# Kernel optimization log

Hardware: AMD Instinct MI355X
Metric: run time of the kernel (lower is better)

The kernel has to match this reference:

```python
import jax, jax.numpy as jnp
import numpy as np

B, S, D, H, L = 64, 512, 512, 512, 2  # batch, seq, input_size, hidden_size, num_layers


def setup_inputs() -> dict:
    key = jax.random.key(0)
    ks = jax.random.split(key, 7)
    scale = 1.0 / np.sqrt(H)  # torch LSTMCell init range
    return {
        "input": jax.random.normal(ks[0], (B, S, D), dtype=jnp.float32),
        "enc_h": jax.random.normal(ks[1], (B, H), dtype=jnp.float32),
        "enc_c": jax.random.normal(ks[2], (B, H), dtype=jnp.float32),
        "W_ih": jax.random.uniform(ks[3], (L, 4 * H, D), jnp.float32, -scale, scale),
        "W_hh": jax.random.uniform(ks[4], (L, 4 * H, H), jnp.float32, -scale, scale),
        "b_ih": jax.random.uniform(ks[5], (L, 4 * H), jnp.float32, -scale, scale),
        "b_hh": jax.random.uniform(ks[6], (L, 4 * H), jnp.float32, -scale, scale),
    }


def _lstm_cell(x, h, c, W_ih_j, W_hh_j, b_ih_j, b_hh_j):
    # PyTorch LSTMCell gate order: i, f, g, o
    gates = x @ W_ih_j.T + b_ih_j + h @ W_hh_j.T + b_hh_j  # [B, 4H]
    i, f, g, o = jnp.split(gates, 4, axis=-1)
    c_new = jax.nn.sigmoid(f) * c + jax.nn.sigmoid(i) * jnp.tanh(g)
    h_new = jax.nn.sigmoid(o) * jnp.tanh(c_new)
    return h_new, c_new


def reference(input, enc_h, enc_c, W_ih, W_hh, b_ih, b_hh):
    # encoder_out is None in this configuration, so attention is skipped;
    # all layers are initialized with (enc_h, enc_c), as in the torch code.
    h0 = jnp.broadcast_to(enc_h, (L,) + enc_h.shape)  # [L, B, H]
    c0 = jnp.broadcast_to(enc_c, (L,) + enc_c.shape)

    def step(carry, x_t):
        hs, cs = carry
        h = x_t
        new_h, new_c = [], []
        for j in range(L):  # small fixed layer loop
            h, c = _lstm_cell(h, hs[j], cs[j], W_ih[j], W_hh[j], b_ih[j], b_hh[j])
            new_h.append(h)
            new_c.append(c)
        return (jnp.stack(new_h), jnp.stack(new_c)), h

    (hs, cs), out = jax.lax.scan(step, (h0, c0), jnp.swapaxes(input, 0, 1))
    out = jnp.swapaxes(out, 0, 1)  # [B, S, H]
    return out, (hs[-1], cs[-1])
```

## Files before the change

### kernel.cpp

```cpp
#include <hip/hip_runtime.h>


#define NB 64
#define NS 512
#define ND 512
#define NH 512

typedef __attribute__((ext_vector_type(8))) short short8;
typedef __attribute__((ext_vector_type(4))) float f32x4;

#define WPK_OFF   0
#define H0_OFF    8388608
#define H1_OFF    8650752
#define FLAGS_OFF 8781824
#define WPK_ELEMS_PER_ROLE (128 * 32 * 512)

__device__ __forceinline__ unsigned int pack2bf(float a, float b) {
    unsigned int ua = __builtin_bit_cast(unsigned int, a);
    unsigned int ub = __builtin_bit_cast(unsigned int, b);
    ua += 0x7fffu + ((ua >> 16) & 1u);
    ub += 0x7fffu + ((ub >> 16) & 1u);
    return (ua >> 16) | (ub & 0xffff0000u);
}
__device__ __forceinline__ unsigned short bf16r(float a) {
    unsigned int ua = __builtin_bit_cast(unsigned int, a);
    ua += 0x7fffu + ((ua >> 16) & 1u);
    return (unsigned short)(ua >> 16);
}

__device__ __forceinline__ unsigned long long ld_h64(const void* p) {
    return __hip_atomic_load((const unsigned long long*)p, __ATOMIC_RELAXED,
                             __HIP_MEMORY_SCOPE_AGENT);
}
__device__ __forceinline__ void st_h32(void* p, unsigned int v) {
    __hip_atomic_store((unsigned int*)p, v, __ATOMIC_RELAXED,
                       __HIP_MEMORY_SCOPE_AGENT);
}
__device__ __forceinline__ unsigned int ld_flag(const unsigned int* p) {
    return __hip_atomic_load(p, __ATOMIC_RELAXED, __HIP_MEMORY_SCOPE_AGENT);
}
__device__ __forceinline__ void st_flag(unsigned int* p, unsigned int v) {
    __hip_atomic_store(p, v, __ATOMIC_RELAXED, __HIP_MEMORY_SCOPE_AGENT);
}

__global__ void prep_weights_k(const float* __restrict__ W_ih,
                               const float* __restrict__ W_hh,
                               unsigned int* __restrict__ wpk_u32) {
    long long gid = (long long)blockIdx.x * blockDim.x + threadIdx.x;
    int l   = (int)(gid & 63);
    int k0i = (int)((gid >> 6) & 31);
    int nt  = (int)((gid >> 11) & 127);
    int r   = (int)(gid >> 18);
    int n = nt * 16 + (l & 15);
    int k = k0i * 32 + ((l >> 4) << 3);
    const float* src;
    if (k < 512) src = W_ih + ((long long)r * 2048 + n) * 512 + k;
    else         src = W_hh + ((long long)r * 2048 + n) * 512 + (k - 512);
    uint4 v;
    v.x = pack2bf(src[0], src[1]);
    v.y = pack2bf(src[2], src[3]);
    v.z = pack2bf(src[4], src[5]);
    v.w = pack2bf(src[6], src[7]);
    ((uint4*)wpk_u32)[gid] = v;
}

__global__ void prep_state_k(const float* __restrict__ eh,
                             unsigned short* __restrict__ h0base,
                             unsigned short* __restrict__ h1base,
                             unsigned int* __restrict__ flags) {
    int i = blockIdx.x * blockDim.x + threadIdx.x;
    if (i < NB * NH) {
        unsigned short hb = bf16r(eh[i]);
        (h0base + 3 * 32768)[i] = hb;
        (h1base + 1 * 32768)[i] = hb;
    }
    if (i < 256) flags[i] = 0;
}

__global__ __launch_bounds__(512, 1)
void lstm_persist_k(const float* __restrict__ input,
                    const float* __restrict__ enc_c,
                    const float* __restrict__ b_ih,
                    const float* __restrict__ b_hh,
                    const unsigned short* __restrict__ wpk,
                    unsigned short* __restrict__ h0base,
                    unsigned short* __restrict__ h1base,
                    float* __restrict__ out,
                    unsigned int* __restrict__ flags) {
    __shared__ alignas(16) unsigned char smem[32768];
    __shared__ float Gp[8][16][17];
    const int bid  = blockIdx.x;
    const int role = bid >> 7;
    const int lb   = bid & 127;
    const int ms   = lb >> 5;
    const int us   = lb & 31;
    const int m0   = ms << 4;
    const int tid  = threadIdx.x;
    const int lane = tid & 63;
    const int w    = tid >> 6;
    const int g    = __builtin_amdgcn_readfirstlane(w & 3);
    const int kh   = __builtin_amdgcn_readfirstlane(w >> 2);

    const unsigned short* wp = wpk + (long long)role * WPK_ELEMS_PER_ROLE
                             + (long long)(g * 32 + us) * (32 * 512)
                             + (long long)kh * 16 * 512;
    const unsigned char* aBase = smem + kh * 16384;

    short8 wreg[16];
    #pragma unroll
    for (int j = 0; j < 16; ++j)
        wreg[j] = *(const short8*)(wp + j * 512 + lane * 8);
    #pragma unroll
    for (int j = 0; j < 16; ++j)
        asm volatile("" : "+v"(wreg[j]));

    unsigned int* myflag   = flags + (ms << 6) + (role << 5) + us;
    const unsigned int* gf = flags + (ms << 6) + lane;

    const int m_l = (tid >> 4) & 15, u_l = tid & 15;
    const int bcell = m0 + m_l;
    const int ucell = us * 16 + u_l;
    float cReg = 0.f, bias_i = 0.f, bias_f = 0.f, bias_g = 0.f, bias_o = 0.f;
    if (tid < 256) {
        cReg = enc_c[bcell * NH + ucell];
        const long long br = (long long)role * 2048;
        bias_i = b_ih[br + 0 * 512 + ucell] + b_hh[br + 0 * 512 + ucell];
        bias_f = b_ih[br + 1 * 512 + ucell] + b_hh[br + 1 * 512 + ucell];
        bias_g = b_ih[br + 2 * 512 + ucell] + b_hh[br + 2 * 512 + ucell];
        bias_o = b_ih[br + 3 * 512 + ucell] + b_hh[br + 3 * 512 + ucell];
    }

    const int srow  = tid & 15;
    const int skoff = ((tid >> 4) & 3) << 3;

    float4 xp[4];
    if (role == 0) {
        #pragma unroll
        for (int j2 = 0; j2 < 2; ++j2) {
            int sid = j2 * 512 + tid;
            int k = (sid >> 6) * 32 + skoff;
            const float* s = input + (long long)(m0 + srow) * (NS * ND) + k;
            xp[2 * j2]     = *(const float4*)s;
            xp[2 * j2 + 1] = *(const float4*)(s + 4);
        }
    }

    for (int i = 0; i <= NS; ++i) {
        const bool active = (role == 0) ? (i < NS) : (i >= 1);

        if (role == 0 && i < NS) {
            #pragma unroll
            for (int j2 = 0; j2 < 2; ++j2) {
                int sid = j2 * 512 + tid;
                float4 lo = xp[2 * j2], hi = xp[2 * j2 + 1];
                uint4 val;
                val.x = pack2bf(lo.x, lo.y);
                val.y = pack2bf(lo.z, lo.w);
                val.z = pack2bf(hi.x, hi.y);
                val.w = pack2bf(hi.z, hi.w);
                *(uint4*)(smem + sid * 16) = val;
            }
        }

        if (i > 0) {
            if (tid < 64) {
                unsigned int thr;
                if (role == 0)
                    thr = (lane < 32) ? (unsigned int)i
                                      : (unsigned int)(i >= 2 ? i - 2 : 0);
                else
                    thr = (unsigned int)i;
                for (;;) {
                    unsigned int v = ld_flag(gf);
                    if (__ballot(v >= thr) == 0xFFFFFFFFFFFFFFFFULL) break;
                    __builtin_amdgcn_s_sleep(1);
                }
            }
            __syncthreads();
        }

        if (active) {
            const unsigned short* h0prev = h0base + (((i - 1) & 3) << 15);
            const unsigned short* hp = (role == 0) ? h0prev
                                     : h1base + ((i & 1) << 15);

            if (role == 1) {
                #pragma unroll
                for (int j2 = 0; j2 < 2; ++j2) {
                    int sid = j2 * 512 + tid;
                    int k = (sid >> 6) * 32 + skoff;
                    const unsigned long long* p =
                        (const unsigned long long*)(h0prev + (long long)(m0 + srow) * 512 + k);
                    unsigned long long lo = ld_h64(p);
                    unsigned long long hi = ld_h64(p + 1);
                    uint4 val;
                    val.x = (unsigned int)lo; val.y = (unsigned int)(lo >> 32);
                    val.z = (unsigned int)hi; val.w = (unsigned int)(hi >> 32);
                    *(uint4*)(smem + sid * 16) = val;
                }
            }
            #pragma unroll
            for (int j2 = 2; j2 < 4; ++j2) {
                int sid = j2 * 512 + tid;
                int k = ((sid >> 6) - 16) * 32 + skoff;
                const unsigned long long* p =
                    (const unsigned long long*)(hp + (long long)(m0 + srow) * 512 + k);
                unsigned long long lo = ld_h64(p);
                unsigned long long hi = ld_h64(p + 1);
                uint4 val;
                val.x = (unsigned int)lo; val.y = (unsigned int)(lo >> 32);
                val.z = (unsigned int)hi; val.w = (unsigned int)(hi >> 32);
                *(uint4*)(smem + sid * 16) = val;
            }
            __syncthreads();

            f32x4 acc0 = {0.f,0.f,0.f,0.f}, acc1 = {0.f,0.f,0.f,0.f};
            #pragma unroll
            for (int j = 0; j < 16; j += 2) {
                short8 a0 = *(const short8*)(aBase + (j + 0) * 1024 + lane * 16);
                short8 a1 = *(const short8*)(aBase + (j + 1) * 1024 + lane * 16);
                acc0 = __builtin_amdgcn_mfma_f32_16x16x32_bf16(a0, wreg[j + 0], acc0, 0, 0, 0);
                acc1 = __builtin_amdgcn_mfma_f32_16x16x32_bf16(a1, wreg[j + 1], acc1, 0, 0, 0);
            }
            f32x4 accS = acc0 + acc1;

            {
                int u_g  = lane & 15;
                int mrow = (lane >> 4) * 4;
                #pragma unroll
                for (int r = 0; r < 4; ++r)
                    Gp[w][mrow + r][u_g] = accS[r];
            }
            __syncthreads();

            if (tid < 256) {
                float gi = Gp[0][m_l][u_l] + Gp[4][m_l][u_l] + bias_i;
                float gf = Gp[1][m_l][u_l] + Gp[5][m_l][u_l] + bias_f;
                float gg = Gp[2][m_l][u_l] + Gp[6][m_l][u_l] + bias_g;
                float go = Gp[3][m_l][u_l] + Gp[7][m_l][u_l] + bias_o;
                float ii = 1.f / (1.f + expf(-gi));
                float ff = 1.f / (1.f + expf(-gf));
                float gv = tanhf(gg);
                float oo = 1.f / (1.f + expf(-go));
                cReg = ff * cReg + ii * gv;
                float hn = oo * tanhf(cReg);

                float hn_p = __shfl_xor(hn, 1);
                if ((u_l & 1) == 0) {
                    unsigned int pk = pack2bf(hn, hn_p);
                    unsigned short* hbuf = (role == 0)
                        ? h0base + ((i & 3) << 15)
                        : h1base + (((i - 1) & 1) << 15);
                    st_h32((unsigned int*)hbuf + ((bcell * NH + ucell) >> 1), pk);
                }
                if (role == 1) {
                    int s = i - 1;
                    out[(long long)bcell * (NS * NH) + (long long)s * NH + ucell] = hn;
                    if (i == NS) {
                        float* dst = out + (long long)NB * NS * NH;
                        dst[bcell * NH + ucell] = hn;
                        dst[NB * NH + bcell * NH + ucell] = cReg;
                    }
                }
            }
        }

        if (i < NS) {
            __syncthreads();
            if (tid == 0) st_flag(myflag, (unsigned int)(i + 1));
            if (role == 0 && i + 1 < NS) {
                #pragma unroll
                for (int j2 = 0; j2 < 2; ++j2) {
                    int sid = j2 * 512 + tid;
                    int k = (sid >> 6) * 32 + skoff;
                    const float* s = input + (long long)(m0 + srow) * (NS * ND)
                                           + (long long)(i + 1) * ND + k;
                    xp[2 * j2]     = *(const float4*)s;
                    xp[2 * j2 + 1] = *(const float4*)(s + 4);
                }
            }
        }
    }
}

extern "C" void kernel_launch(void* const* d_in, const int* in_sizes, int n_in,
                              void* d_out, int out_size, void* d_ws, size_t ws_size,
                              hipStream_t stream) {
    const float* input = (const float*)d_in[0];
    const float* enc_h = (const float*)d_in[1];
    const float* enc_c = (const float*)d_in[2];
    const float* W_ih  = (const float*)d_in[3];
    const float* W_hh  = (const float*)d_in[4];
    const float* b_ih  = (const float*)d_in[5];
    const float* b_hh  = (const float*)d_in[6];
    float* out = (float*)d_out;
    unsigned char* ws = (unsigned char*)d_ws;

    unsigned short* wpk    = (unsigned short*)(ws + WPK_OFF);
    unsigned short* h0base = (unsigned short*)(ws + H0_OFF);
    unsigned short* h1base = (unsigned short*)(ws + H1_OFF);
    unsigned int*   flags  = (unsigned int*)(ws + FLAGS_OFF);

    prep_weights_k<<<2048, 256, 0, stream>>>(W_ih, W_hh, (unsigned int*)wpk);
    prep_state_k<<<128, 256, 0, stream>>>(enc_h, h0base, h1base, flags);
    lstm_persist_k<<<256, 512, 0, stream>>>(input, enc_c, b_ih, b_hh, wpk,
                                            h0base, h1base, out, flags);
}
```

Before: 2.020 ms.

## Replace flag-based data handoff with step-tagged hidden-state words polled directly

Hidden states are now stored as 32-bit words pairing a bf16 value with a step tag, in 8-deep ring buffers. Consumers poll the data itself with uncached loads until every tag matches the expected step, so the per-step wait on hidden data no longer needs the flag round trip and block-wide barrier. Flags are still kept for the write-after-read guard and are now posted right after the gate reduction, and the next input prefetch moves earlier. The cost is twice the bytes per hidden-state load and store, spin loops on every wave, and reliance on 32-bit stores being seen atomically.

```diff
diff --git a/kernel.cpp b/kernel.cpp
--- a/kernel.cpp
+++ b/kernel.cpp
@@ -8,11 +8,12 @@
 
 typedef __attribute__((ext_vector_type(8))) short short8;
 typedef __attribute__((ext_vector_type(4))) float f32x4;
+typedef __attribute__((ext_vector_type(4))) unsigned int u32x4;
 
 #define WPK_OFF   0
-#define H0_OFF    8388608
-#define H1_OFF    8650752
-#define FLAGS_OFF 8781824
+#define HT0_OFF   8388608
+#define HT1_OFF   9437184
+#define FLAGS_OFF 10485760
 #define WPK_ELEMS_PER_ROLE (128 * 32 * 512)
 
 __device__ __forceinline__ unsigned int pack2bf(float a, float b) {
@@ -28,19 +29,43 @@
     return (unsigned short)(ua >> 16);
 }
 
-__device__ __forceinline__ unsigned long long ld_h64(const void* p) {
-    return __hip_atomic_load((const unsigned long long*)p, __ATOMIC_RELAXED,
-                             __HIP_MEMORY_SCOPE_AGENT);
-}
-__device__ __forceinline__ void st_h32(void* p, unsigned int v) {
-    __hip_atomic_store((unsigned int*)p, v, __ATOMIC_RELAXED,
-                       __HIP_MEMORY_SCOPE_AGENT);
+__device__ __forceinline__ void st_h32(unsigned int* p, unsigned int v) {
+    __hip_atomic_store(p, v, __ATOMIC_RELAXED, __HIP_MEMORY_SCOPE_AGENT);
 }
 __device__ __forceinline__ unsigned int ld_flag(const unsigned int* p) {
     return __hip_atomic_load(p, __ATOMIC_RELAXED, __HIP_MEMORY_SCOPE_AGENT);
 }
 __device__ __forceinline__ void st_flag(unsigned int* p, unsigned int v) {
     __hip_atomic_store(p, v, __ATOMIC_RELAXED, __HIP_MEMORY_SCOPE_AGENT);
+}
+
+__device__ __forceinline__ bool tag8_ok(const u32x4& a, const u32x4& b, unsigned int T) {
+    unsigned int m = ((a.x >> 16) ^ T) | ((a.y >> 16) ^ T)
+                   | ((a.z >> 16) ^ T) | ((a.w >> 16) ^ T)
+                   | ((b.x >> 16) ^ T) | ((b.y >> 16) ^ T)
+                   | ((b.z >> 16) ^ T) | ((b.w >> 16) ^ T);
+    return m == 0;
+}
+__device__ __forceinline__ u32x4 pack8(const u32x4& a, const u32x4& b) {
+    u32x4 r;
+    r.x = (a.x & 0xFFFFu) | (a.y << 16);
+    r.y = (a.z & 0xFFFFu) | (a.w << 16);
+    r.z = (b.x & 0xFFFFu) | (b.y << 16);
+    r.w = (b.z & 0xFFFFu) | (b.w << 16);
+    return r;
+}
+
+__device__ __forceinline__ void load2(const unsigned int* q0, const unsigned int* q1,
+                                      u32x4& a0, u32x4& b0, u32x4& a1, u32x4& b1) {
+    asm volatile(
+        "global_load_dwordx4 %0, %4, off sc0 sc1\n\t"
+        "global_load_dwordx4 %1, %4, off offset:16 sc0 sc1\n\t"
+        "global_load_dwordx4 %2, %5, off sc0 sc1\n\t"
+        "global_load_dwordx4 %3, %5, off offset:16 sc0 sc1\n\t"
+        "s_waitcnt vmcnt(0)"
+        : "=&v"(a0), "=&v"(b0), "=&v"(a1), "=&v"(b1)
+        : "v"(q0), "v"(q1) : "memory");
+    __builtin_amdgcn_sched_barrier(0);
 }
 
 __global__ void prep_weights_k(const float* __restrict__ W_ih,
@@ -65,16 +90,17 @@
 }
 
 __global__ void prep_state_k(const float* __restrict__ eh,
-                             unsigned short* __restrict__ h0base,
-                             unsigned short* __restrict__ h1base,
+                             unsigned int* __restrict__ ht0,
+                             unsigned int* __restrict__ ht1,
                              unsigned int* __restrict__ flags) {
-    int i = blockIdx.x * blockDim.x + threadIdx.x;
-    if (i < NB * NH) {
-        unsigned short hb = bf16r(eh[i]);
-        (h0base + 3 * 32768)[i] = hb;
-        (h1base + 1 * 32768)[i] = hb;
+    int gid = blockIdx.x * blockDim.x + threadIdx.x;
+    if (gid < 262144) {
+        int buf = gid >> 15, idx = gid & 32767;
+        unsigned int v = (buf == 7) ? (unsigned int)bf16r(eh[idx]) : 0u;
+        ht0[gid] = v;
+        ht1[gid] = v;
     }
-    if (i < 256) flags[i] = 0;
+    if (gid < 256) flags[gid] = 0;
 }
 
 __global__ __launch_bounds__(512, 1)
@@ -83,8 +109,8 @@
                     const float* __restrict__ b_ih,
                     const float* __restrict__ b_hh,
                     const unsigned short* __restrict__ wpk,
-                    unsigned short* __restrict__ h0base,
-                    unsigned short* __restrict__ h1base,
+                    unsigned int* __restrict__ ht0,
+                    unsigned int* __restrict__ ht1,
                     float* __restrict__ out,
                     unsigned int* __restrict__ flags) {
     __shared__ alignas(16) unsigned char smem[32768];
@@ -132,6 +158,8 @@
 
     const int srow  = tid & 15;
     const int skoff = ((tid >> 4) & 3) << 3;
+    const int w32   = w << 5;
+    const int rowoff = (m0 + srow) * 512 + w32 + skoff;
 
     float4 xp[4];
     if (role == 0) {
@@ -163,54 +191,52 @@
         }
 
         if (i > 0) {
-            if (tid < 64) {
-                unsigned int thr;
-                if (role == 0)
-                    thr = (lane < 32) ? (unsigned int)i
-                                      : (unsigned int)(i >= 2 ? i - 2 : 0);
-                else
-                    thr = (unsigned int)i;
+            unsigned int thr;
+            if (role == 0)
+                thr = (lane < 32) ? (unsigned int)i
+                                  : (unsigned int)(i >= 2 ? i - 2 : 0);
+            else
+                thr = (unsigned int)i;
+            for (;;) {
+                unsigned int v = ld_flag(gf);
+                if (__ballot(v >= thr) == 0xFFFFFFFFFFFFFFFFULL) break;
+                __builtin_amdgcn_s_sleep(1);
+            }
+        }
+
+        if (active) {
+            if (role == 0) {
+                const unsigned int* hb = ht0 + (((i - 1) & 7) << 15);
+                const unsigned int T = (unsigned int)i;
+                const unsigned int* q0 = hb + rowoff;
+                const unsigned int* q1 = q0 + 256;
+                u32x4 a0, b0, a1, b1;
                 for (;;) {
-                    unsigned int v = ld_flag(gf);
-                    if (__ballot(v >= thr) == 0xFFFFFFFFFFFFFFFFULL) break;
-                    __builtin_amdgcn_s_sleep(1);
+                    load2(q0, q1, a0, b0, a1, b1);
+                    if (tag8_ok(a0, b0, T) && tag8_ok(a1, b1, T)) break;
                 }
-            }
-            __syncthreads();
-        }
-
-        if (active) {
-            const unsigned short* h0prev = h0base + (((i - 1) & 3) << 15);
-            const unsigned short* hp = (role == 0) ? h0prev
-                                     : h1base + ((i & 1) << 15);
-
-            if (role == 1) {
-                #pragma unroll
-                for (int j2 = 0; j2 < 2; ++j2) {
-                    int sid = j2 * 512 + tid;
-                    int k = (sid >> 6) * 32 + skoff;
-                    const unsigned long long* p =
-                        (const unsigned long long*)(h0prev + (long long)(m0 + srow) * 512 + k);
-                    unsigned long long lo = ld_h64(p);
-                    unsigned long long hi = ld_h64(p + 1);
-                    uint4 val;
-                    val.x = (unsigned int)lo; val.y = (unsigned int)(lo >> 32);
-                    val.z = (unsigned int)hi; val.w = (unsigned int)(hi >> 32);
-                    *(uint4*)(smem + sid * 16) = val;
+                *(u32x4*)(smem + (1024 + tid) * 16) = pack8(a0, b0);
+                *(u32x4*)(smem + (1536 + tid) * 16) = pack8(a1, b1);
+            } else {
+                const unsigned int* xb = ht0 + (((i - 1) & 7) << 15);
+                const unsigned int* hb = ht1 + (((i - 2) & 7) << 15);
+                const unsigned int Tx = (unsigned int)i;
+                const unsigned int Th = (unsigned int)(i - 1);
+                const unsigned int* px0 = xb + rowoff;
+                const unsigned int* px1 = px0 + 256;
+                const unsigned int* ph0 = hb + rowoff;
+                const unsigned int* ph1 = ph0 + 256;
+                u32x4 xa0, xc0, xa1, xc1, ha0, hc0, ha1, hc1;
+                for (;;) {
+                    load2(px0, px1, xa0, xc0, xa1, xc1);
+                    load2(ph0, ph1, ha0, hc0, ha1, hc1);
+                    if (tag8_ok(xa0, xc0, Tx) && tag8_ok(xa1, xc1, Tx) &&
+                        tag8_ok(ha0, hc0, Th) && tag8_ok(ha1, hc1, Th)) break;
                 }
-            }
-            #pragma unroll
-            for (int j2 = 2; j2 < 4; ++j2) {
-                int sid = j2 * 512 + tid;
-                int k = ((sid >> 6) - 16) * 32 + skoff;
-                const unsigned long long* p =
-                    (const unsigned long long*)(hp + (long long)(m0 + srow) * 512 + k);
-                unsigned long long lo = ld_h64(p);
-                unsigned long long hi = ld_h64(p + 1);
-                uint4 val;
-                val.x = (unsigned int)lo; val.y = (unsigned int)(lo >> 32);
-                val.z = (unsigned int)hi; val.w = (unsigned int)(hi >> 32);
-                *(uint4*)(smem + sid * 16) = val;
+                *(u32x4*)(smem + (tid) * 16)        = pack8(xa0, xc0);
+                *(u32x4*)(smem + (512 + tid) * 16)  = pack8(xa1, xc1);
+                *(u32x4*)(smem + (1024 + tid) * 16) = pack8(ha0, hc0);
+                *(u32x4*)(smem + (1536 + tid) * 16) = pack8(ha1, hc1);
             }
             __syncthreads();
 
@@ -223,7 +249,6 @@
                 acc1 = __builtin_amdgcn_mfma_f32_16x16x32_bf16(a1, wreg[j + 1], acc1, 0, 0, 0);
             }
             f32x4 accS = acc0 + acc1;
-
             {
                 int u_g  = lane & 15;
                 int mrow = (lane >> 4) * 4;
@@ -232,6 +257,20 @@
                     Gp[w][mrow + r][u_g] = accS[r];
             }
             __syncthreads();
+
+            if (tid == 0) st_flag(myflag, (unsigned int)(i + 1));
+
+            if (role == 0 && i + 1 < NS) {
+                #pragma unroll
+                for (int j2 = 0; j2 < 2; ++j2) {
+                    int sid = j2 * 512 + tid;
+                    int k = (sid >> 6) * 32 + skoff;
+                    const float* s = input + (long long)(m0 + srow) * (NS * ND)
+                                           + (long long)(i + 1) * ND + k;
+                    xp[2 * j2]     = *(const float4*)s;
+                    xp[2 * j2 + 1] = *(const float4*)(s + 4);
+                }
+            }
 
             if (tid < 256) {
                 float gi = Gp[0][m_l][u_l] + Gp[4][m_l][u_l] + bias_i;
@@ -244,16 +283,16 @@
                 float oo = 1.f / (1.f + expf(-go));
                 cReg = ff * cReg + ii * gv;
                 float hn = oo * tanhf(cReg);
-
-                float hn_p = __shfl_xor(hn, 1);
-                if ((u_l & 1) == 0) {
-                    unsigned int pk = pack2bf(hn, hn_p);
-                    unsigned short* hbuf = (role == 0)
-                        ? h0base + ((i & 3) << 15)
-                        : h1base + (((i - 1) & 1) << 15);
-                    st_h32((unsigned int*)hbuf + ((bcell * NH + ucell) >> 1), pk);
-                }
-                if (role == 1) {
+                unsigned short hb16 = bf16r(hn);
+
+                if (role == 0) {
+                    unsigned int* hbuf = ht0 + ((i & 7) << 15);
+                    st_h32(hbuf + bcell * 512 + ucell,
+                           ((unsigned int)(i + 1) << 16) | hb16);
+                } else {
+                    unsigned int* hbuf = ht1 + (((i - 1) & 7) << 15);
+                    st_h32(hbuf + bcell * 512 + ucell,
+                           ((unsigned int)i << 16) | hb16);
                     int s = i - 1;
                     out[(long long)bcell * (NS * NH) + (long long)s * NH + ucell] = hn;
                     if (i == NS) {
@@ -263,22 +302,8 @@
                     }
                 }
             }
-        }
-
-        if (i < NS) {
-            __syncthreads();
+        } else {
             if (tid == 0) st_flag(myflag, (unsigned int)(i + 1));
-            if (role == 0 && i + 1 < NS) {
-                #pragma unroll
-                for (int j2 = 0; j2 < 2; ++j2) {
-                    int sid = j2 * 512 + tid;
-                    int k = (sid >> 6) * 32 + skoff;
-                    const float* s = input + (long long)(m0 + srow) * (NS * ND)
-                                           + (long long)(i + 1) * ND + k;
-                    xp[2 * j2]     = *(const float4*)s;
-                    xp[2 * j2 + 1] = *(const float4*)(s + 4);
-                }
-            }
         }
     }
 }
@@ -296,13 +321,13 @@
     float* out = (float*)d_out;
     unsigned char* ws = (unsigned char*)d_ws;
 
-    unsigned short* wpk    = (unsigned short*)(ws + WPK_OFF);
-    unsigned short* h0base = (unsigned short*)(ws + H0_OFF);
-    unsigned short* h1base = (unsigned short*)(ws + H1_OFF);
-    unsigned int*   flags  = (unsigned int*)(ws + FLAGS_OFF);
+    unsigned short* wpk   = (unsigned short*)(ws + WPK_OFF);
+    unsigned int*   ht0   = (unsigned int*)(ws + HT0_OFF);
+    unsigned int*   ht1   = (unsigned int*)(ws + HT1_OFF);
+    unsigned int*   flags = (unsigned int*)(ws + FLAGS_OFF);
 
     prep_weights_k<<<2048, 256, 0, stream>>>(W_ih, W_hh, (unsigned int*)wpk);
-    prep_state_k<<<128, 256, 0, stream>>>(enc_h, h0base, h1base, flags);
+    prep_state_k<<<1024, 256, 0, stream>>>(enc_h, ht0, ht1, flags);
     lstm_persist_k<<<256, 512, 0, stream>>>(input, enc_c, b_ih, b_hh, wpk,
-                                            h0base, h1base, out, flags);
-}
+                                            ht0, ht1, out, flags);
+}
```

Result: slower. 2.657 ms (+31.6%).

## Per-wave K-split with direct global fragment loads and fine-grained per-wave flags

Applied to the files above, without the earlier changes.

Restructures the persistent LSTM kernel so each wave owns a K slice across all four gates and loads its bf16 A fragments straight from global memory into registers, dropping the shared-memory staging buffer and its barriers. Dependencies become per-wave flags polled with a vector load and no sleep, so each wave waits only on the producers of its own K slice. Gate partials go into a double-buffered LDS array, leaving one block barrier per step. The h1 ring grows to four slots and the flag area moves to make room. The cost is more flag polling traffic, cross-wave reduction over eight partials, and subtle memory-ordering assumptions in the inline-asm loads and stores.

```diff
diff --git a/kernel.cpp b/kernel.cpp
--- a/kernel.cpp
+++ b/kernel.cpp
@@ -8,11 +8,12 @@
 
 typedef __attribute__((ext_vector_type(8))) short short8;
 typedef __attribute__((ext_vector_type(4))) float f32x4;
+typedef __attribute__((ext_vector_type(4))) unsigned int u32x4;
 
 #define WPK_OFF   0
 #define H0_OFF    8388608
 #define H1_OFF    8650752
-#define FLAGS_OFF 8781824
+#define FLAGS_OFF 8912896
 #define WPK_ELEMS_PER_ROLE (128 * 32 * 512)
 
 __device__ __forceinline__ unsigned int pack2bf(float a, float b) {
@@ -28,19 +29,32 @@
     return (unsigned short)(ua >> 16);
 }
 
-__device__ __forceinline__ unsigned long long ld_h64(const void* p) {
-    return __hip_atomic_load((const unsigned long long*)p, __ATOMIC_RELAXED,
-                             __HIP_MEMORY_SCOPE_AGENT);
-}
-__device__ __forceinline__ void st_h32(void* p, unsigned int v) {
-    __hip_atomic_store((unsigned int*)p, v, __ATOMIC_RELAXED,
-                       __HIP_MEMORY_SCOPE_AGENT);
-}
-__device__ __forceinline__ unsigned int ld_flag(const unsigned int* p) {
-    return __hip_atomic_load(p, __ATOMIC_RELAXED, __HIP_MEMORY_SCOPE_AGENT);
+__device__ __forceinline__ void st_h32(unsigned int* p, unsigned int v) {
+    __hip_atomic_store(p, v, __ATOMIC_RELAXED, __HIP_MEMORY_SCOPE_AGENT);
 }
 __device__ __forceinline__ void st_flag(unsigned int* p, unsigned int v) {
     __hip_atomic_store(p, v, __ATOMIC_RELAXED, __HIP_MEMORY_SCOPE_AGENT);
+}
+
+__device__ __forceinline__ u32x4 ld_flags4(const unsigned int* p) {
+    u32x4 r;
+    asm volatile("global_load_dwordx4 %0, %1, off sc0 sc1\n\ts_waitcnt vmcnt(0)"
+                 : "=&v"(r) : "v"(p) : "memory");
+    return r;
+}
+__device__ __forceinline__ void ld4x16(const unsigned short* p0, const unsigned short* p1,
+                                       const unsigned short* p2, const unsigned short* p3,
+                                       short8& a0, short8& a1, short8& a2, short8& a3) {
+    asm volatile(
+        "global_load_dwordx4 %0, %4, off sc0 sc1\n\t"
+        "global_load_dwordx4 %1, %5, off sc0 sc1\n\t"
+        "global_load_dwordx4 %2, %6, off sc0 sc1\n\t"
+        "global_load_dwordx4 %3, %7, off sc0 sc1\n\t"
+        "s_waitcnt vmcnt(0)"
+        : "=&v"(a0), "=&v"(a1), "=&v"(a2), "=&v"(a3)
+        : "v"(p0), "v"(p1), "v"(p2), "v"(p3)
+        : "memory");
+    __builtin_amdgcn_sched_barrier(0);
 }
 
 __global__ void prep_weights_k(const float* __restrict__ W_ih,
@@ -72,9 +86,9 @@
     if (i < NB * NH) {
         unsigned short hb = bf16r(eh[i]);
         (h0base + 3 * 32768)[i] = hb;
-        (h1base + 1 * 32768)[i] = hb;
-    }
-    if (i < 256) flags[i] = 0;
+        (h1base + 3 * 32768)[i] = hb;
+    }
+    if (i < 1024) flags[i] = 0;
 }
 
 __global__ __launch_bounds__(512, 1)
@@ -87,8 +101,8 @@
                     unsigned short* __restrict__ h1base,
                     float* __restrict__ out,
                     unsigned int* __restrict__ flags) {
-    __shared__ alignas(16) unsigned char smem[32768];
-    __shared__ float Gp[8][16][17];
+    __shared__ float Gp[2][8][4][16][17];
+
     const int bid  = blockIdx.x;
     const int role = bid >> 7;
     const int lb   = bid & 127;
@@ -97,25 +111,36 @@
     const int m0   = ms << 4;
     const int tid  = threadIdx.x;
     const int lane = tid & 63;
-    const int w    = tid >> 6;
-    const int g    = __builtin_amdgcn_readfirstlane(w & 3);
-    const int kh   = __builtin_amdgcn_readfirstlane(w >> 2);
-
-    const unsigned short* wp = wpk + (long long)role * WPK_ELEMS_PER_ROLE
-                             + (long long)(g * 32 + us) * (32 * 512)
-                             + (long long)kh * 16 * 512;
-    const unsigned char* aBase = smem + kh * 16384;
+    const int w    = __builtin_amdgcn_readfirstlane(tid >> 6);
+    const int wh   = (w >= 4) ? (w - 4) : 0;
+
+    const int row  = m0 + (lane & 15);
+    const int col8 = (lane >> 4) << 3;
 
     short8 wreg[16];
     #pragma unroll
-    for (int j = 0; j < 16; ++j)
-        wreg[j] = *(const short8*)(wp + j * 512 + lane * 8);
+    for (int g2 = 0; g2 < 4; ++g2)
+        #pragma unroll
+        for (int jj = 0; jj < 4; ++jj)
+            wreg[g2 * 4 + jj] = *(const short8*)(wpk
+                + (long long)role * WPK_ELEMS_PER_ROLE
+                + (long long)(g2 * 32 + us) * (32 * 512)
+                + (long long)(w * 4 + jj) * 512 + lane * 8);
     #pragma unroll
     for (int j = 0; j < 16; ++j)
         asm volatile("" : "+v"(wreg[j]));
 
-    unsigned int* myflag   = flags + (ms << 6) + (role << 5) + us;
-    const unsigned int* gf = flags + (ms << 6) + lane;
+    unsigned int* fb = flags + (ms << 8);
+    unsigned int* myflag = fb + role * 128 + us * 4 + w;
+    const unsigned int* pollp;
+    {
+        int idx;
+        if (role == 0)      idx = (lane < 8) ? (wh * 32 + lane * 4)
+                                : (lane < 40 ? (128 + (lane - 8) * 4) : ((lane & 7) * 4));
+        else if (w < 4)     idx = (lane < 8) ? (w * 32 + lane * 4) : ((lane & 7) * 4);
+        else                idx = (lane < 8) ? (128 + wh * 32 + lane * 4) : (128 + (lane & 7) * 4);
+        pollp = fb + idx;
+    }
 
     const int m_l = (tid >> 4) & 15, u_l = tid & 15;
     const int bcell = m0 + m_l;
@@ -130,153 +155,125 @@
         bias_o = b_ih[br + 3 * 512 + ucell] + b_hh[br + 3 * 512 + ucell];
     }
 
-    const int srow  = tid & 15;
-    const int skoff = ((tid >> 4) & 3) << 3;
-
-    float4 xp[4];
-    if (role == 0) {
+    float4 xpA[4], xpB[4];
+    if (role == 0 && w < 4) {
         #pragma unroll
-        for (int j2 = 0; j2 < 2; ++j2) {
-            int sid = j2 * 512 + tid;
-            int k = (sid >> 6) * 32 + skoff;
-            const float* s = input + (long long)(m0 + srow) * (NS * ND) + k;
-            xp[2 * j2]     = *(const float4*)s;
-            xp[2 * j2 + 1] = *(const float4*)(s + 4);
+        for (int jj = 0; jj < 4; ++jj) {
+            const float* s = input + (long long)row * (NS * ND)
+                                   + (w * 4 + jj) * 32 + col8;
+            xpA[jj] = *(const float4*)s;
+            xpB[jj] = *(const float4*)(s + 4);
         }
     }
 
     for (int i = 0; i <= NS; ++i) {
+        const int par = i & 1;
         const bool active = (role == 0) ? (i < NS) : (i >= 1);
 
-        if (role == 0 && i < NS) {
+        if (active) {
+            short8 a[4];
+            if (role == 0 && w < 4) {
+                #pragma unroll
+                for (int jj = 0; jj < 4; ++jj) {
+                    u32x4 u;
+                    u.x = pack2bf(xpA[jj].x, xpA[jj].y);
+                    u.y = pack2bf(xpA[jj].z, xpA[jj].w);
+                    u.z = pack2bf(xpB[jj].x, xpB[jj].y);
+                    u.w = pack2bf(xpB[jj].z, xpB[jj].w);
+                    a[jj] = __builtin_bit_cast(short8, u);
+                }
+            } else {
+                unsigned thr;
+                if (role == 0)
+                    thr = (lane < 8) ? (unsigned)i
+                        : (lane < 40 ? (unsigned)(i >= 2 ? i - 2 : 0) : 0u);
+                else if (w < 4)
+                    thr = (lane < 8) ? (unsigned)i : 0u;
+                else
+                    thr = (lane < 8 && i >= 2) ? (unsigned)i : 0u;
+                for (;;) {
+                    u32x4 f = ld_flags4(pollp);
+                    unsigned mn  = f.x < f.y ? f.x : f.y;
+                    unsigned mn2 = f.z < f.w ? f.z : f.w;
+                    mn = mn < mn2 ? mn : mn2;
+                    if (__ballot(mn >= thr) == 0xFFFFFFFFFFFFFFFFULL) break;
+                }
+                const unsigned short* hsrc;
+                int ubase;
+                if (role == 0)      { hsrc = h0base + (((i - 1) & 3) << 15); ubase = wh * 128; }
+                else if (w < 4)     { hsrc = h0base + (((i - 1) & 3) << 15); ubase = w * 128; }
+                else                { hsrc = h1base + (((i - 2) & 3) << 15); ubase = wh * 128; }
+                const unsigned short* pr = hsrc + row * 512 + ubase + col8;
+                ld4x16(pr, pr + 32, pr + 64, pr + 96, a[0], a[1], a[2], a[3]);
+            }
+
+            f32x4 acc[4];
             #pragma unroll
-            for (int j2 = 0; j2 < 2; ++j2) {
-                int sid = j2 * 512 + tid;
-                float4 lo = xp[2 * j2], hi = xp[2 * j2 + 1];
-                uint4 val;
-                val.x = pack2bf(lo.x, lo.y);
-                val.y = pack2bf(lo.z, lo.w);
-                val.z = pack2bf(hi.x, hi.y);
-                val.w = pack2bf(hi.z, hi.w);
-                *(uint4*)(smem + sid * 16) = val;
+            for (int g2 = 0; g2 < 4; ++g2) acc[g2] = (f32x4){0.f, 0.f, 0.f, 0.f};
+            #pragma unroll
+            for (int jj = 0; jj < 4; ++jj)
+                #pragma unroll
+                for (int g2 = 0; g2 < 4; ++g2)
+                    acc[g2] = __builtin_amdgcn_mfma_f32_16x16x32_bf16(
+                        a[jj], wreg[g2 * 4 + jj], acc[g2], 0, 0, 0);
+
+            {
+                int rbase = (lane >> 4) * 4, cidx = lane & 15;
+                #pragma unroll
+                for (int g2 = 0; g2 < 4; ++g2)
+                    #pragma unroll
+                    for (int r = 0; r < 4; ++r)
+                        Gp[par][w][g2][rbase + r][cidx] = acc[g2][r];
             }
         }
 
-        if (i > 0) {
-            if (tid < 64) {
-                unsigned int thr;
-                if (role == 0)
-                    thr = (lane < 32) ? (unsigned int)i
-                                      : (unsigned int)(i >= 2 ? i - 2 : 0);
-                else
-                    thr = (unsigned int)i;
-                for (;;) {
-                    unsigned int v = ld_flag(gf);
-                    if (__ballot(v >= thr) == 0xFFFFFFFFFFFFFFFFULL) break;
-                    __builtin_amdgcn_s_sleep(1);
+        __syncthreads();
+
+        if (active && tid < 256) {
+            float s0 = bias_i, s1 = bias_f, s2 = bias_g, s3 = bias_o;
+            #pragma unroll
+            for (int w8 = 0; w8 < 8; ++w8) {
+                s0 += Gp[par][w8][0][m_l][u_l];
+                s1 += Gp[par][w8][1][m_l][u_l];
+                s2 += Gp[par][w8][2][m_l][u_l];
+                s3 += Gp[par][w8][3][m_l][u_l];
+            }
+            float ii = 1.f / (1.f + expf(-s0));
+            float ff = 1.f / (1.f + expf(-s1));
+            float gv = tanhf(s2);
+            float oo = 1.f / (1.f + expf(-s3));
+            cReg = ff * cReg + ii * gv;
+            float hn = oo * tanhf(cReg);
+
+            float hn_p = __shfl_xor(hn, 1);
+            unsigned short* hbuf = (role == 0)
+                ? h0base + ((i & 3) << 15)
+                : h1base + (((i - 1) & 3) << 15);
+            if ((u_l & 1) == 0)
+                st_h32((unsigned int*)hbuf + ((bcell * 512 + ucell) >> 1),
+                       pack2bf(hn, hn_p));
+            __builtin_amdgcn_sched_barrier(0);
+            asm volatile("s_waitcnt vmcnt(0)" ::: "memory");
+            __builtin_amdgcn_sched_barrier(0);
+            if (lane == 0) st_flag(myflag, (unsigned int)(i + 1));
+
+            if (role == 1) {
+                int s = i - 1;
+                out[(long long)bcell * (NS * NH) + (long long)s * NH + ucell] = hn;
+                if (i == NS) {
+                    float* dst = out + (long long)NB * NS * NH;
+                    dst[bcell * NH + ucell] = hn;
+                    dst[NB * NH + bcell * NH + ucell] = cReg;
                 }
             }
-            __syncthreads();
-        }
-
-        if (active) {
-            const unsigned short* h0prev = h0base + (((i - 1) & 3) << 15);
-            const unsigned short* hp = (role == 0) ? h0prev
-                                     : h1base + ((i & 1) << 15);
-
-            if (role == 1) {
-                #pragma unroll
-                for (int j2 = 0; j2 < 2; ++j2) {
-                    int sid = j2 * 512 + tid;
-                    int k = (sid >> 6) * 32 + skoff;
-                    const unsigned long long* p =
-                        (const unsigned long long*)(h0prev + (long long)(m0 + srow) * 512 + k);
-                    unsigned long long lo = ld_h64(p);
-                    unsigned long long hi = ld_h64(p + 1);
-                    uint4 val;
-                    val.x = (unsigned int)lo; val.y = (unsigned int)(lo >> 32);
-                    val.z = (unsigned int)hi; val.w = (unsigned int)(hi >> 32);
-                    *(uint4*)(smem + sid * 16) = val;
-                }
-            }
-            #pragma unroll
-            for (int j2 = 2; j2 < 4; ++j2) {
-                int sid = j2 * 512 + tid;
-                int k = ((sid >> 6) - 16) * 32 + skoff;
-                const unsigned long long* p =
-                    (const unsigned long long*)(hp + (long long)(m0 + srow) * 512 + k);
-                unsigned long long lo = ld_h64(p);
-                unsigned long long hi = ld_h64(p + 1);
-                uint4 val;
-                val.x = (unsigned int)lo; val.y = (unsigned int)(lo >> 32);
-                val.z = (unsigned int)hi; val.w = (unsigned int)(hi >> 32);
-                *(uint4*)(smem + sid * 16) = val;
-            }
-            __syncthreads();
-
-            f32x4 acc0 = {0.f,0.f,0.f,0.f}, acc1 = {0.f,0.f,0.f,0.f};
-            #pragma unroll
-            for (int j = 0; j < 16; j += 2) {
-                short8 a0 = *(const short8*)(aBase + (j + 0) * 1024 + lane * 16);
-                short8 a1 = *(const short8*)(aBase + (j + 1) * 1024 + lane * 16);
-                acc0 = __builtin_amdgcn_mfma_f32_16x16x32_bf16(a0, wreg[j + 0], acc0, 0, 0, 0);
-                acc1 = __builtin_amdgcn_mfma_f32_16x16x32_bf16(a1, wreg[j + 1], acc1, 0, 0, 0);
-            }
-            f32x4 accS = acc0 + acc1;
-
-            {
-                int u_g  = lane & 15;
-                int mrow = (lane >> 4) * 4;
-                #pragma unroll
-                for (int r = 0; r < 4; ++r)
-                    Gp[w][mrow + r][u_g] = accS[r];
-            }
-            __syncthreads();
-
-            if (tid < 256) {
-                float gi = Gp[0][m_l][u_l] + Gp[4][m_l][u_l] + bias_i;
-                float gf = Gp[1][m_l][u_l] + Gp[5][m_l][u_l] + bias_f;
-                float gg = Gp[2][m_l][u_l] + Gp[6][m_l][u_l] + bias_g;
-                float go = Gp[3][m_l][u_l] + Gp[7][m_l][u_l] + bias_o;
-                float ii = 1.f / (1.f + expf(-gi));
-                float ff = 1.f / (1.f + expf(-gf));
-                float gv = tanhf(gg);
-                float oo = 1.f / (1.f + expf(-go));
-                cReg = ff * cReg + ii * gv;
-                float hn = oo * tanhf(cReg);
-
-                float hn_p = __shfl_xor(hn, 1);
-                if ((u_l & 1) == 0) {
-                    unsigned int pk = pack2bf(hn, hn_p);
-                    unsigned short* hbuf = (role == 0)
-                        ? h0base + ((i & 3) << 15)
-                        : h1base + (((i - 1) & 1) << 15);
-                    st_h32((unsigned int*)hbuf + ((bcell * NH + ucell) >> 1), pk);
-                }
-                if (role == 1) {
-                    int s = i - 1;
-                    out[(long long)bcell * (NS * NH) + (long long)s * NH + ucell] = hn;
-                    if (i == NS) {
-                        float* dst = out + (long long)NB * NS * NH;
-                        dst[bcell * NH + ucell] = hn;
-                        dst[NB * NH + bcell * NH + ucell] = cReg;
-                    }
-                }
-            }
-        }
-
-        if (i < NS) {
-            __syncthreads();
-            if (tid == 0) st_flag(myflag, (unsigned int)(i + 1));
             if (role == 0 && i + 1 < NS) {
                 #pragma unroll
-                for (int j2 = 0; j2 < 2; ++j2) {
-                    int sid = j2 * 512 + tid;
-                    int k = (sid >> 6) * 32 + skoff;
-                    const float* s = input + (long long)(m0 + srow) * (NS * ND)
-                                           + (long long)(i + 1) * ND + k;
-                    xp[2 * j2]     = *(const float4*)s;
-                    xp[2 * j2 + 1] = *(const float4*)(s + 4);
+                for (int jj = 0; jj < 4; ++jj) {
+                    const float* s = input + (long long)row * (NS * ND)
+                                           + (long long)(i + 1) * ND
+                                           + (w * 4 + jj) * 32 + col8;
+                    xpA[jj] = *(const float4*)s;
+                    xpB[jj] = *(const float4*)(s + 4);
                 }
             }
         }
```

After: 3.205 ms. 1.59x slower.

## Replace per-block step flags with per-wave flags polled by every wave

Applied to the files above, without the earlier changes.

Each compute wave now publishes its own step flag as soon as its h-state stores drain, using s_waitcnt vmcnt(0). This replaces the block-wide __syncthreads plus the single flag from thread 0. Every wave polls 256 flags with dwordx4 system-coherent loads instead of one wave polling and then hitting a barrier. The intent is to cut two block barriers per timestep from the serial recurrence critical path. The cost is more polling traffic on the flag lines and reliance on the cross-block flag protocol for intra-block smem reuse ordering.

```diff
diff --git a/kernel.cpp b/kernel.cpp
--- a/kernel.cpp
+++ b/kernel.cpp
@@ -8,6 +8,8 @@
 
 typedef __attribute__((ext_vector_type(8))) short short8;
 typedef __attribute__((ext_vector_type(4))) float f32x4;
+typedef __attribute__((ext_vector_type(4))) unsigned int u32x4;
+typedef unsigned long long ull;
 
 #define WPK_OFF   0
 #define H0_OFF    8388608
@@ -28,19 +30,20 @@
     return (unsigned short)(ua >> 16);
 }
 
-__device__ __forceinline__ unsigned long long ld_h64(const void* p) {
-    return __hip_atomic_load((const unsigned long long*)p, __ATOMIC_RELAXED,
-                             __HIP_MEMORY_SCOPE_AGENT);
+__device__ __forceinline__ ull ld_h64(const void* p) {
+    return __hip_atomic_load((const ull*)p, __ATOMIC_RELAXED, __HIP_MEMORY_SCOPE_AGENT);
 }
 __device__ __forceinline__ void st_h32(void* p, unsigned int v) {
-    __hip_atomic_store((unsigned int*)p, v, __ATOMIC_RELAXED,
-                       __HIP_MEMORY_SCOPE_AGENT);
-}
-__device__ __forceinline__ unsigned int ld_flag(const unsigned int* p) {
-    return __hip_atomic_load(p, __ATOMIC_RELAXED, __HIP_MEMORY_SCOPE_AGENT);
+    __hip_atomic_store((unsigned int*)p, v, __ATOMIC_RELAXED, __HIP_MEMORY_SCOPE_AGENT);
 }
 __device__ __forceinline__ void st_flag(unsigned int* p, unsigned int v) {
     __hip_atomic_store(p, v, __ATOMIC_RELAXED, __HIP_MEMORY_SCOPE_AGENT);
+}
+__device__ __forceinline__ u32x4 ld_flags4(const unsigned int* p) {
+    u32x4 r;
+    asm volatile("global_load_dwordx4 %0, %1, off sc0 sc1\n\ts_waitcnt vmcnt(0)"
+                 : "=&v"(r) : "v"(p) : "memory");
+    return r;
 }
 
 __global__ void prep_weights_k(const float* __restrict__ W_ih,
@@ -74,7 +77,7 @@
         (h0base + 3 * 32768)[i] = hb;
         (h1base + 1 * 32768)[i] = hb;
     }
-    if (i < 256) flags[i] = 0;
+    if (i < 1024) flags[i] = 0;
 }
 
 __global__ __launch_bounds__(512, 1)
@@ -114,8 +117,9 @@
     for (int j = 0; j < 16; ++j)
         asm volatile("" : "+v"(wreg[j]));
 
-    unsigned int* myflag   = flags + (ms << 6) + (role << 5) + us;
-    const unsigned int* gf = flags + (ms << 6) + lane;
+    unsigned int* fb = flags + (ms << 8);
+    unsigned int* myflagw = fb + (role << 7) + (us << 2) + w;
+    const unsigned int* pollp = fb + (lane << 2);
 
     const int m_l = (tid >> 4) & 15, u_l = tid & 15;
     const int bcell = m0 + m_l;
@@ -148,22 +152,22 @@
     for (int i = 0; i <= NS; ++i) {
         const bool active = (role == 0) ? (i < NS) : (i >= 1);
 
-        if (role == 0 && i < NS) {
-            #pragma unroll
-            for (int j2 = 0; j2 < 2; ++j2) {
-                int sid = j2 * 512 + tid;
-                float4 lo = xp[2 * j2], hi = xp[2 * j2 + 1];
-                uint4 val;
-                val.x = pack2bf(lo.x, lo.y);
-                val.y = pack2bf(lo.z, lo.w);
-                val.z = pack2bf(hi.x, hi.y);
-                val.w = pack2bf(hi.z, hi.w);
-                *(uint4*)(smem + sid * 16) = val;
-            }
-        }
-
-        if (i > 0) {
-            if (tid < 64) {
+        if (active) {
+            if (role == 0) {
+                #pragma unroll
+                for (int j2 = 0; j2 < 2; ++j2) {
+                    int sid = j2 * 512 + tid;
+                    float4 lo = xp[2 * j2], hi = xp[2 * j2 + 1];
+                    uint4 val;
+                    val.x = pack2bf(lo.x, lo.y);
+                    val.y = pack2bf(lo.z, lo.w);
+                    val.z = pack2bf(hi.x, hi.y);
+                    val.w = pack2bf(hi.z, hi.w);
+                    *(uint4*)(smem + sid * 16) = val;
+                }
+            }
+
+            if (i > 0) {
                 unsigned int thr;
                 if (role == 0)
                     thr = (lane < 32) ? (unsigned int)i
@@ -171,15 +175,15 @@
                 else
                     thr = (unsigned int)i;
                 for (;;) {
-                    unsigned int v = ld_flag(gf);
-                    if (__ballot(v >= thr) == 0xFFFFFFFFFFFFFFFFULL) break;
+                    u32x4 f = ld_flags4(pollp);
+                    unsigned int mn  = f.x < f.y ? f.x : f.y;
+                    unsigned int mn2 = f.z < f.w ? f.z : f.w;
+                    mn = mn < mn2 ? mn : mn2;
+                    if (__ballot(mn >= thr) == 0xFFFFFFFFFFFFFFFFULL) break;
                     __builtin_amdgcn_s_sleep(1);
                 }
             }
-            __syncthreads();
-        }
-
-        if (active) {
+
             const unsigned short* h0prev = h0base + (((i - 1) & 3) << 15);
             const unsigned short* hp = (role == 0) ? h0prev
                                      : h1base + ((i & 1) << 15);
@@ -189,10 +193,9 @@
                 for (int j2 = 0; j2 < 2; ++j2) {
                     int sid = j2 * 512 + tid;
                     int k = (sid >> 6) * 32 + skoff;
-                    const unsigned long long* p =
-                        (const unsigned long long*)(h0prev + (long long)(m0 + srow) * 512 + k);
-                    unsigned long long lo = ld_h64(p);
-                    unsigned long long hi = ld_h64(p + 1);
+                    const ull* p = (const ull*)(h0prev + (long long)(m0 + srow) * 512 + k);
+                    ull lo = ld_h64(p);
+                    ull hi = ld_h64(p + 1);
                     uint4 val;
                     val.x = (unsigned int)lo; val.y = (unsigned int)(lo >> 32);
                     val.z = (unsigned int)hi; val.w = (unsigned int)(hi >> 32);
@@ -203,10 +206,9 @@
             for (int j2 = 2; j2 < 4; ++j2) {
                 int sid = j2 * 512 + tid;
                 int k = ((sid >> 6) - 16) * 32 + skoff;
-                const unsigned long long* p =
-                    (const unsigned long long*)(hp + (long long)(m0 + srow) * 512 + k);
-                unsigned long long lo = ld_h64(p);
-                unsigned long long hi = ld_h64(p + 1);
+                const ull* p = (const ull*)(hp + (long long)(m0 + srow) * 512 + k);
+                ull lo = ld_h64(p);
+                ull hi = ld_h64(p + 1);
                 uint4 val;
                 val.x = (unsigned int)lo; val.y = (unsigned int)(lo >> 32);
                 val.z = (unsigned int)hi; val.w = (unsigned int)(hi >> 32);
@@ -223,7 +225,6 @@
                 acc1 = __builtin_amdgcn_mfma_f32_16x16x32_bf16(a1, wreg[j + 1], acc1, 0, 0, 0);
             }
             f32x4 accS = acc0 + acc1;
-
             {
                 int u_g  = lane & 15;
                 int mrow = (lane >> 4) * 4;
@@ -234,14 +235,14 @@
             __syncthreads();
 
             if (tid < 256) {
-                float gi = Gp[0][m_l][u_l] + Gp[4][m_l][u_l] + bias_i;
-                float gf = Gp[1][m_l][u_l] + Gp[5][m_l][u_l] + bias_f;
-                float gg = Gp[2][m_l][u_l] + Gp[6][m_l][u_l] + bias_g;
-                float go = Gp[3][m_l][u_l] + Gp[7][m_l][u_l] + bias_o;
-                float ii = 1.f / (1.f + expf(-gi));
-                float ff = 1.f / (1.f + expf(-gf));
-                float gv = tanhf(gg);
-                float oo = 1.f / (1.f + expf(-go));
+                float s0 = Gp[0][m_l][u_l] + Gp[4][m_l][u_l] + bias_i;
+                float s1 = Gp[1][m_l][u_l] + Gp[5][m_l][u_l] + bias_f;
+                float s2 = Gp[2][m_l][u_l] + Gp[6][m_l][u_l] + bias_g;
+                float s3 = Gp[3][m_l][u_l] + Gp[7][m_l][u_l] + bias_o;
+                float ii = 1.f / (1.f + expf(-s0));
+                float ff = 1.f / (1.f + expf(-s1));
+                float gv = tanhf(s2);
+                float oo = 1.f / (1.f + expf(-s3));
                 cReg = ff * cReg + ii * gv;
                 float hn = oo * tanhf(cReg);
 
@@ -253,6 +254,11 @@
                         : h1base + (((i - 1) & 1) << 15);
                     st_h32((unsigned int*)hbuf + ((bcell * NH + ucell) >> 1), pk);
                 }
+                __builtin_amdgcn_sched_barrier(0);
+                asm volatile("s_waitcnt vmcnt(0)" ::: "memory");
+                __builtin_amdgcn_sched_barrier(0);
+                if (lane == 0) st_flag(myflagw, (unsigned int)(i + 1));
+
                 if (role == 1) {
                     int s = i - 1;
                     out[(long long)bcell * (NS * NH) + (long long)s * NH + ucell] = hn;
@@ -262,23 +268,32 @@
                         dst[NB * NH + bcell * NH + ucell] = cReg;
                     }
                 }
-            }
-        }
-
-        if (i < NS) {
-            __syncthreads();
-            if (tid == 0) st_flag(myflag, (unsigned int)(i + 1));
-            if (role == 0 && i + 1 < NS) {
-                #pragma unroll
-                for (int j2 = 0; j2 < 2; ++j2) {
-                    int sid = j2 * 512 + tid;
-                    int k = (sid >> 6) * 32 + skoff;
-                    const float* s = input + (long long)(m0 + srow) * (NS * ND)
-                                           + (long long)(i + 1) * ND + k;
-                    xp[2 * j2]     = *(const float4*)s;
-                    xp[2 * j2 + 1] = *(const float4*)(s + 4);
-                }
-            }
+                if (role == 0 && i + 1 < NS) {
+                    #pragma unroll
+                    for (int j2 = 0; j2 < 2; ++j2) {
+                        int sid = j2 * 512 + tid;
+                        int k = (sid >> 6) * 32 + skoff;
+                        const float* s = input + (long long)(m0 + srow) * (NS * ND)
+                                               + (long long)(i + 1) * ND + k;
+                        xp[2 * j2]     = *(const float4*)s;
+                        xp[2 * j2 + 1] = *(const float4*)(s + 4);
+                    }
+                }
+            } else {
+                if (role == 0 && i + 1 < NS) {
+                    #pragma unroll
+                    for (int j2 = 0; j2 < 2; ++j2) {
+                        int sid = j2 * 512 + tid;
+                        int k = (sid >> 6) * 32 + skoff;
+                        const float* s = input + (long long)(m0 + srow) * (NS * ND)
+                                               + (long long)(i + 1) * ND + k;
+                        xp[2 * j2]     = *(const float4*)s;
+                        xp[2 * j2 + 1] = *(const float4*)(s + 4);
+                    }
+                }
+            }
+        } else {
+            if (tid < 256 && lane == 0) st_flag(myflagw, (unsigned int)(i + 1));
         }
     }
 }
```

After: 4.656 ms. 2.31x slower.
